# Kernel tuning notes

Measured on AMD Instinct MI355X. Metric: run time of the kernel, lower is better.

The kernel has to match this reference:

```python
import jax, jax.numpy as jnp
import numpy as np

B, T, D = 2, 2048, 1024
H = 16
HD = D // H  # 64


def setup_inputs() -> dict:
    key = jax.random.key(0)
    k1, k2, k3, k4, k5 = jax.random.split(key, 5)
    s = 0.02
    return {
        "x": jax.random.normal(k1, (B, T, D), dtype=jnp.float32),
        "Wqkv": jax.random.normal(k2, (D, 3 * D), dtype=jnp.float32) * s,
        "bqkv": jax.random.normal(k3, (3 * D,), dtype=jnp.float32) * s,
        "Wout": jax.random.normal(k4, (D, D), dtype=jnp.float32) * s,
        "bout": jax.random.normal(k5, (D,), dtype=jnp.float32) * s,
    }


def reference(x, Wqkv, bqkv, Wout, bout):
    b, t, c = x.shape
    qkv = (x @ Wqkv + bqkv).reshape(b, t, 3, H, HD)
    q = jnp.transpose(qkv[:, :, 0], (0, 2, 1, 3))  # [B,H,T,HD]
    k = jnp.transpose(qkv[:, :, 1], (0, 2, 1, 3))
    v = jnp.transpose(qkv[:, :, 2], (0, 2, 1, 3))
    att = jnp.einsum("bhqd,bhkd->bhqk", q, k) * (HD ** -0.5)
    mask = jnp.tril(jnp.ones((t, t), dtype=bool))  # causal, no past kv
    att = jnp.where(mask, att, -jnp.inf)
    att = jax.nn.softmax(att, axis=-1)
    y = jnp.einsum("bhqk,bhkd->bhqd", att, v)
    y = jnp.transpose(y, (0, 2, 1, 3)).reshape(b, t, c)
    return y @ Wout + bout
```

## Files before the change

kernel.cpp:

```cpp
#include <hip/hip_runtime.h>
#include <hip/hip_bf16.h>
#include <math.h>

#define B_  2
#define T_  2048
#define D_  1024
#define H_  16
#define HD_ 64

typedef __attribute__((ext_vector_type(8))) short short8;
typedef __attribute__((ext_vector_type(4))) float f32x4;

#if __has_builtin(__builtin_amdgcn_exp2f)
#define EXP2F __builtin_amdgcn_exp2f
#else
#define EXP2F exp2f
#endif

__device__ __forceinline__ ushort f2bf(float x) {
    unsigned u = __builtin_bit_cast(unsigned, x);
    return (ushort)((u + 0x7FFFu + ((u >> 16) & 1u)) >> 16);
}

__device__ __forceinline__ unsigned pack_bf2_fast(float a, float b) {
    unsigned ua = __builtin_bit_cast(unsigned, a) + 0x8000u;
    unsigned ub = __builtin_bit_cast(unsigned, b) + 0x8000u;
    return (ua >> 16) | (ub & 0xFFFF0000u);
}

__device__ __forceinline__ void load_lds_16B(const ushort* g, ushort* l) {
    __builtin_amdgcn_global_load_lds(
        (const __attribute__((address_space(1))) unsigned*)g,
        (__attribute__((address_space(3))) unsigned*)l, 16, 0, 0);
}

__global__ __launch_bounds__(256)
void prep_kernel(const float* __restrict__ x, ushort* __restrict__ xb,
                 const float* __restrict__ Wqkv, ushort* __restrict__ Wqkvt,
                 const float* __restrict__ Wout, ushort* __restrict__ Woutt)
{
    __shared__ ushort Ts[64][65];
    const int bid = blockIdx.x;

    if (bid < 512) {
        const int n4 = (B_ * T_ * D_) / 4;
        for (int i = bid * 256 + threadIdx.x; i < n4; i += 512 * 256) {
            float4 v = ((const float4*)x)[i];
            ushort4 o = { f2bf(v.x), f2bf(v.y), f2bf(v.z), f2bf(v.w) };
            ((ushort4*)xb)[i] = o;
        }
        return;
    }

    const float* W; ushort* Wt; int K, M, m0, k0;
    if (bid < 1280) {
        const int t = bid - 512;
        W = Wqkv; Wt = Wqkvt; K = D_; M = 3 * D_;
        m0 = (t % 48) * 64; k0 = (t / 48) * 64;
    } else {
        const int t = bid - 1280;
        W = Wout; Wt = Woutt; K = D_; M = D_;
        m0 = (t % 16) * 64; k0 = (t / 16) * 64;
    }

    const int tr = threadIdx.x >> 4;
    const int tc = threadIdx.x & 15;
    #pragma unroll
    for (int it = 0; it < 4; it++) {
        int k = tr + it * 16;
        float4 v = *(const float4*)&W[(size_t)(k0 + k) * M + m0 + tc * 4];
        Ts[tc * 4 + 0][k] = f2bf(v.x);
        Ts[tc * 4 + 1][k] = f2bf(v.y);
        Ts[tc * 4 + 2][k] = f2bf(v.z);
        Ts[tc * 4 + 3][k] = f2bf(v.w);
    }
    __syncthreads();
    #pragma unroll
    for (int it = 0; it < 2; it++) {
        const int mr  = (threadIdx.x >> 3) + it * 32;
        const int seg = (threadIdx.x & 7) * 8;
        short8 v;
        #pragma unroll
        for (int r = 0; r < 8; r++) v[r] = (short)Ts[mr][seg + r];
        *(short8*)&Wt[(size_t)(m0 + mr) * K + k0 + seg] = v;
    }
}

__global__ __launch_bounds__(256, 4)
void gemm_qkv(const ushort* __restrict__ A, const ushort* __restrict__ Bt,
              const float* __restrict__ bias,
              ushort* __restrict__ Qg, ushort* __restrict__ Kg,
              ushort* __restrict__ Vtg)
{
    const int K = D_;
    __shared__ __align__(16) ushort lds[16384];
    ushort* Asl = lds;
    ushort* Bsl = lds + 8192;

    const int tid = threadIdx.x;
    const int w  = tid >> 6, L = tid & 63;
    const int lt = L & 15, lq = L >> 4;
    const int wr = w >> 1, wc = w & 1;
    const int m0 = blockIdx.x * 128, n0 = blockIdx.y * 128;
    const int rsub = L >> 3;
    const int pgr  = L & 7;

    f32x4 acc[4][4] = {};

    for (int k0 = 0; k0 < K; k0 += 64) {
        __syncthreads();
        #pragma unroll
        for (int j = 0; j < 4; j++) {
            const int row  = (w * 4 + j) * 8 + rsub;
            const int gran = pgr ^ rsub;
            load_lds_16B(A  + (size_t)(n0 + row) * K + k0 + gran * 8,
                         &Asl[row * 64 + pgr * 8]);
            load_lds_16B(Bt + (size_t)(m0 + row) * K + k0 + gran * 8,
                         &Bsl[row * 64 + pgr * 8]);
        }
        __syncthreads();

        #pragma unroll
        for (int ks = 0; ks < 2; ks++) {
            short8 af[4], bf[4];
            #pragma unroll
            for (int i = 0; i < 4; i++) {
                const int ra = wr * 64 + i * 16 + lt;
                af[i] = *(const short8*)&Asl[ra * 64 + (((ks * 4 + lq) ^ (ra & 7)) * 8)];
                const int rb = wc * 64 + i * 16 + lt;
                bf[i] = *(const short8*)&Bsl[rb * 64 + (((ks * 4 + lq) ^ (rb & 7)) * 8)];
            }
            #pragma unroll
            for (int i = 0; i < 4; i++)
                #pragma unroll
                for (int j = 0; j < 4; j++)
                    acc[i][j] = __builtin_amdgcn_mfma_f32_16x16x32_bf16(af[i], bf[j], acc[i][j], 0, 0, 0);
        }
    }

    __syncthreads();
    const int s  = m0 >> 10;
    const int h0 = (m0 & 1023) >> 6;
    const float qs = (s == 0) ? 0.18033688011112042f : 1.0f;

    if (s < 2) {
        #pragma unroll
        for (int j = 0; j < 4; j++) {
            const int m  = wc * 64 + j * 16 + lt;
            const float bv = bias[m0 + m];
            #pragma unroll
            for (int i = 0; i < 4; i++) {
                const int n = wr * 64 + i * 16 + lq * 4;
                #pragma unroll
                for (int r = 0; r < 4; r++)
                    lds[(n + r) * 128 + m] = f2bf((acc[i][j][r] + bv) * qs);
            }
        }
        __syncthreads();
        ushort* dst = (s == 0 ? Qg : Kg);
        #pragma unroll
        for (int it = 0; it < 8; it++) {
            const int g   = tid + it * 256;
            const int row = g >> 4, c = g & 15;
            const int n = n0 + row;
            const int b = n >> 11, t = n & 2047;
            const int h = h0 + (c >> 3), d = (c & 7) * 8;
            short8 v = *(const short8*)&lds[row * 128 + c * 8];
            *(short8*)&dst[((size_t)(b * H_ + h) * T_ + t) * HD_ + d] = v;
        }
    } else {
        #pragma unroll
        for (int j = 0; j < 4; j++) {
            const int m  = wc * 64 + j * 16 + lt;
            const float bv = bias[m0 + m];
            #pragma unroll
            for (int i = 0; i < 4; i++) {
                const int n = wr * 64 + i * 16 + lq * 4;
                uint2 pk = { pack_bf2_fast(acc[i][j][0] + bv, acc[i][j][1] + bv),
                             pack_bf2_fast(acc[i][j][2] + bv, acc[i][j][3] + bv) };
                *(uint2*)&lds[m * 128 + n] = pk;
            }
        }
        __syncthreads();
        const int b = n0 >> 11, t0 = n0 & 2047;
        #pragma unroll
        for (int it = 0; it < 8; it++) {
            const int g   = tid + it * 256;
            const int row = g >> 4, c = g & 15;
            const int h = h0 + (row >> 6), d = row & 63;
            short8 v = *(const short8*)&lds[row * 128 + c * 8];
            *(short8*)&Vtg[((size_t)(b * H_ + h) * HD_ + d) * T_ + t0 + c * 8] = v;
        }
    }
}

__global__ __launch_bounds__(256, 4)
void gemm_out(const ushort* __restrict__ A, const ushort* __restrict__ Bt,
              const float* __restrict__ bias, float* __restrict__ C)
{
    const int K = D_, M = D_;
    __shared__ __align__(16) ushort lds[8192 + 4096];
    ushort* Asl = lds;
    ushort* Bsl = lds + 8192;

    const int tid = threadIdx.x;
    const int w  = tid >> 6, L = tid & 63;
    const int lt = L & 15, lq = L >> 4;
    const int wr = w >> 1, wc = w & 1;
    const int m0 = blockIdx.x * 64, n0 = blockIdx.y * 128;
    const int rsub = L >> 3;
    const int pgr  = L & 7;

    f32x4 acc[2][4] = {};

    for (int k0 = 0; k0 < K; k0 += 64) {
        __syncthreads();
        #pragma unroll
        for (int j = 0; j < 4; j++) {
            const int row  = (w * 4 + j) * 8 + rsub;
            const int gran = pgr ^ rsub;
            load_lds_16B(A + (size_t)(n0 + row) * K + k0 + gran * 8,
                         &Asl[row * 64 + pgr * 8]);
        }
        #pragma unroll
        for (int j = 0; j < 2; j++) {
            const int row  = (w * 2 + j) * 8 + rsub;
            const int gran = pgr ^ rsub;
            load_lds_16B(Bt + (size_t)(m0 + row) * K + k0 + gran * 8,
                         &Bsl[row * 64 + pgr * 8]);
        }
        __syncthreads();

        #pragma unroll
        for (int ks = 0; ks < 2; ks++) {
            short8 wf[2], yf[4];
            #pragma unroll
            for (int j = 0; j < 2; j++) {
                const int rb = wc * 32 + j * 16 + lt;
                wf[j] = *(const short8*)&Bsl[rb * 64 + (((ks * 4 + lq) ^ (rb & 7)) * 8)];
            }
            #pragma unroll
            for (int i = 0; i < 4; i++) {
                const int ra = wr * 64 + i * 16 + lt;
                yf[i] = *(const short8*)&Asl[ra * 64 + (((ks * 4 + lq) ^ (ra & 7)) * 8)];
            }
            #pragma unroll
            for (int j = 0; j < 2; j++)
                #pragma unroll
                for (int i = 0; i < 4; i++)
                    acc[j][i] = __builtin_amdgcn_mfma_f32_16x16x32_bf16(wf[j], yf[i], acc[j][i], 0, 0, 0);
        }
    }

    #pragma unroll
    for (int j = 0; j < 2; j++) {
        const int mbase = m0 + wc * 32 + j * 16 + lq * 4;
        const float4 bv = *(const float4*)&bias[mbase];
        #pragma unroll
        for (int i = 0; i < 4; i++) {
            const int n = n0 + wr * 64 + i * 16 + lt;
            float4 o = { acc[j][i][0] + bv.x, acc[j][i][1] + bv.y,
                         acc[j][i][2] + bv.z, acc[j][i][3] + bv.w };
            *(float4*)&C[(size_t)n * M + mbase] = o;
        }
    }
}

__global__ __launch_bounds__(256, 4)
void attn_mfma(const ushort* __restrict__ Qg, const ushort* __restrict__ Kg,
               const ushort* __restrict__ Vtg, ushort* __restrict__ yb)
{
    const int h = blockIdx.y, b = blockIdx.z;
    const int flip = ((blockIdx.y >> 3) ^ blockIdx.z) & 1;
    const int qb = flip ? blockIdx.x : (31 - blockIdx.x);
    const int tid = threadIdx.x;
    const int w  = tid >> 6, L = tid & 63;
    const int lt = L & 15, lq = L >> 4;
    const int kswz = lt & 7;

    __shared__ __align__(16) ushort Ks [128 * 64];
    __shared__ __align__(16) ushort Vts[64 * 128];
    __shared__ __align__(16) ushort Ps [4][16 * 40];

    const size_t bh = (size_t)(b * H_ + h);
    const ushort* Qbase  = Qg  + bh * T_ * HD_;
    const ushort* Kbase  = Kg  + bh * T_ * HD_;
    const ushort* Vtbase = Vtg + bh * HD_ * T_;

    const int q_glob = qb * 64 + w * 16 + lt;
    const short8 qf0 = *(const short8*)(Qbase + (size_t)q_glob * HD_ + lq * 8);
    const short8 qf1 = *(const short8*)(Qbase + (size_t)q_glob * HD_ + 32 + lq * 8);

    f32x4 acc_o[4] = {};
    float lsum = 0.f;

    const int krow = tid >> 3, kpg = tid & 7;
    const int vrow = tid >> 4, vpg = tid & 15;
    const int nk = (qb + 2) >> 1;

    for (int kb = 0; kb < nk; kb++) {
        __syncthreads();
        #pragma unroll
        for (int rr = 0; rr < 4; rr++) {
            const int row = krow + 32 * rr;
            load_lds_16B(Kbase + (size_t)(kb * 128 + row) * HD_ + (kpg ^ (row & 7)) * 8,
                         &Ks[row * 64 + kpg * 8]);
        }
        #pragma unroll
        for (int rr = 0; rr < 4; rr++) {
            const int d = vrow + 16 * rr;
            load_lds_16B(Vtbase + (size_t)d * T_ + kb * 128 + (vpg ^ (d & 7)) * 8,
                         &Vts[d * 128 + vpg * 8]);
        }
        __syncthreads();

        if (kb < nk - 1) {
            #pragma unroll
            for (int ks = 0; ks < 4; ks++) {
                const int row0 = (2 * ks) * 16 + lt;
                const int row1 = row0 + 16;
                short8 a00 = *(const short8*)&Ks[row0 * 64 + ((lq ^ kswz) * 8)];
                short8 a01 = *(const short8*)&Ks[row0 * 64 + (((4 + lq) ^ kswz) * 8)];
                short8 a10 = *(const short8*)&Ks[row1 * 64 + ((lq ^ kswz) * 8)];
                short8 a11 = *(const short8*)&Ks[row1 * 64 + (((4 + lq) ^ kswz) * 8)];
                f32x4 c0 = {}, c1 = {};
                c0 = __builtin_amdgcn_mfma_f32_16x16x32_bf16(a00, qf0, c0, 0, 0, 0);
                c0 = __builtin_amdgcn_mfma_f32_16x16x32_bf16(a01, qf1, c0, 0, 0, 0);
                c1 = __builtin_amdgcn_mfma_f32_16x16x32_bf16(a10, qf0, c1, 0, 0, 0);
                c1 = __builtin_amdgcn_mfma_f32_16x16x32_bf16(a11, qf1, c1, 0, 0, 0);

                float p0 = EXP2F(c0[0]), p1 = EXP2F(c0[1]);
                float p2 = EXP2F(c0[2]), p3 = EXP2F(c0[3]);
                float p4 = EXP2F(c1[0]), p5 = EXP2F(c1[1]);
                float p6 = EXP2F(c1[2]), p7 = EXP2F(c1[3]);
                lsum += ((p0 + p1) + (p2 + p3)) + ((p4 + p5) + (p6 + p7));
                uint2 pk0 = { pack_bf2_fast(p0, p1), pack_bf2_fast(p2, p3) };
                uint2 pk1 = { pack_bf2_fast(p4, p5), pack_bf2_fast(p6, p7) };
                *(uint2*)&Ps[w][lt * 40 + lq * 4]      = pk0;
                *(uint2*)&Ps[w][lt * 40 + 16 + lq * 4] = pk1;

                short8 pf = *(const short8*)&Ps[w][lt * 40 + lq * 8];

                #pragma unroll
                for (int dt = 0; dt < 4; dt++) {
                    const int vr = dt * 16 + lt;
                    short8 vf = *(const short8*)&Vts[vr * 128 + (((ks * 4 + lq) ^ kswz) * 8)];
                    acc_o[dt] = __builtin_amdgcn_mfma_f32_16x16x32_bf16(pf, vf, acc_o[dt], 0, 0, 0);
                }
            }
        } else {
            const int ksN = (qb & 1) ? 4 : 2;
            const int mk0 = (qb & 1) ? 2 : 0;
            for (int ks = 0; ks < ksN; ks++) {
                const int row0 = (2 * ks) * 16 + lt;
                const int row1 = row0 + 16;
                short8 a00 = *(const short8*)&Ks[row0 * 64 + ((lq ^ kswz) * 8)];
                short8 a01 = *(const short8*)&Ks[row0 * 64 + (((4 + lq) ^ kswz) * 8)];
                short8 a10 = *(const short8*)&Ks[row1 * 64 + ((lq ^ kswz) * 8)];
                short8 a11 = *(const short8*)&Ks[row1 * 64 + (((4 + lq) ^ kswz) * 8)];
                f32x4 c0 = {}, c1 = {};
                c0 = __builtin_amdgcn_mfma_f32_16x16x32_bf16(a00, qf0, c0, 0, 0, 0);
                c0 = __builtin_amdgcn_mfma_f32_16x16x32_bf16(a01, qf1, c0, 0, 0, 0);
                c1 = __builtin_amdgcn_mfma_f32_16x16x32_bf16(a10, qf0, c1, 0, 0, 0);
                c1 = __builtin_amdgcn_mfma_f32_16x16x32_bf16(a11, qf1, c1, 0, 0, 0);

                float p[8];
                #pragma unroll
                for (int r = 0; r < 4; r++) { p[r] = EXP2F(c0[r]); p[4 + r] = EXP2F(c1[r]); }
                if (ks >= mk0) {
                    const int key0 = kb * 128 + (2 * ks) * 16 + lq * 4;
                    #pragma unroll
                    for (int r = 0; r < 4; r++) {
                        if (key0 + r > q_glob)      p[r] = 0.f;
                        if (key0 + 16 + r > q_glob) p[4 + r] = 0.f;
                    }
                }
                lsum += ((p[0] + p[1]) + (p[2] + p[3])) + ((p[4] + p[5]) + (p[6] + p[7]));
                uint2 pk0 = { pack_bf2_fast(p[0], p[1]), pack_bf2_fast(p[2], p[3]) };
                uint2 pk1 = { pack_bf2_fast(p[4], p[5]), pack_bf2_fast(p[6], p[7]) };
                *(uint2*)&Ps[w][lt * 40 + lq * 4]      = pk0;
                *(uint2*)&Ps[w][lt * 40 + 16 + lq * 4] = pk1;

                short8 pf = *(const short8*)&Ps[w][lt * 40 + lq * 8];

                #pragma unroll
                for (int dt = 0; dt < 4; dt++) {
                    const int vr = dt * 16 + lt;
                    short8 vf = *(const short8*)&Vts[vr * 128 + (((ks * 4 + lq) ^ kswz) * 8)];
                    acc_o[dt] = __builtin_amdgcn_mfma_f32_16x16x32_bf16(pf, vf, acc_o[dt], 0, 0, 0);
                }
            }
        }
    }

    lsum += __shfl_xor(lsum, 16, 64);
    lsum += __shfl_xor(lsum, 32, 64);
    const float inv = 1.0f / lsum;

    float linv[4];
    #pragma unroll
    for (int r = 0; r < 4; r++) linv[r] = __shfl(inv, lq * 4 + r, 64);

    ushort* ybase = yb + (size_t)(b * T_ + qb * 64 + w * 16) * D_ + h * HD_;
    #pragma unroll
    for (int r = 0; r < 4; r++)
        #pragma unroll
        for (int dt = 0; dt < 4; dt++)
            ybase[(size_t)(lq * 4 + r) * D_ + dt * 16 + lt] = f2bf(acc_o[dt][r] * linv[r]);
}

extern "C" void kernel_launch(void* const* d_in, const int* in_sizes, int n_in,
                              void* d_out, int out_size, void* d_ws, size_t ws_size,
                              hipStream_t stream)
{
    const float* x    = (const float*)d_in[0];
    const float* Wqkv = (const float*)d_in[1];
    const float* bqkv = (const float*)d_in[2];
    const float* Wout = (const float*)d_in[3];
    const float* bout = (const float*)d_in[4];
    float* out = (float*)d_out;

    char* ws = (char*)d_ws;
    const size_t NT = (size_t)B_ * T_;
    ushort* xb     = (ushort*)ws;
    ushort* Wqkvt  = (ushort*)(ws + NT * D_ * 2);
    ushort* Woutt  = (ushort*)(ws + NT * D_ * 2 + (size_t)3 * D_ * D_ * 2);
    char*   p      = ws + NT * D_ * 2 + (size_t)4 * D_ * D_ * 2;
    const size_t qkv_elems = (size_t)B_ * H_ * T_ * HD_;
    ushort* Qg  = (ushort*)p;
    ushort* Kg  = (ushort*)(p + qkv_elems * 2);
    ushort* Vtg = (ushort*)(p + qkv_elems * 4);
    ushort* yb  = (ushort*)(p + qkv_elems * 6);

    prep_kernel<<<1536, 256, 0, stream>>>(x, xb, Wqkv, Wqkvt, Wout, Woutt);

    gemm_qkv<<<dim3(3 * D_ / 128, NT / 128), 256, 0, stream>>>(
        xb, Wqkvt, bqkv, Qg, Kg, Vtg);

    attn_mfma<<<dim3(32, H_, B_), 256, 0, stream>>>(Qg, Kg, Vtg, yb);

    gemm_out<<<dim3(D_ / 64, NT / 128), 256, 0, stream>>>(
        yb, Woutt, bout, out);
}
```

Before: 168.9 us.

## Process 128 query rows per attention block to reuse K/V tiles

Each attention block now covers 128 query rows instead of 64, with every wavefront handling two 16-row query sub-tiles. Each K/V tile staged in LDS therefore feeds twice as many MFMAs, halving the global K/V traffic and barrier count per query. The P scratch buffer is double-buffered per sub-tile and the diagonal block uses per-sub-tile causal masking. The cost is higher register pressure (launch bounds lowered to 2 blocks), half as many blocks (512) and a coarser load-balancing flip between batches.

```diff
diff --git a/kernel.cpp b/kernel.cpp
--- a/kernel.cpp
+++ b/kernel.cpp
@@ -266,13 +266,12 @@
     }
 }
 
-__global__ __launch_bounds__(256, 4)
+__global__ __launch_bounds__(256, 2)
 void attn_mfma(const ushort* __restrict__ Qg, const ushort* __restrict__ Kg,
                const ushort* __restrict__ Vtg, ushort* __restrict__ yb)
 {
     const int h = blockIdx.y, b = blockIdx.z;
-    const int flip = ((blockIdx.y >> 3) ^ blockIdx.z) & 1;
-    const int qb = flip ? blockIdx.x : (31 - blockIdx.x);
+    const int Qt = blockIdx.z ? blockIdx.x : (15 - blockIdx.x);
     const int tid = threadIdx.x;
     const int w  = tid >> 6, L = tid & 63;
     const int lt = L & 15, lq = L >> 4;
@@ -280,23 +279,27 @@
 
     __shared__ __align__(16) ushort Ks [128 * 64];
     __shared__ __align__(16) ushort Vts[64 * 128];
-    __shared__ __align__(16) ushort Ps [4][16 * 40];
+    __shared__ __align__(16) ushort Ps [4][2][2][640];
 
     const size_t bh = (size_t)(b * H_ + h);
     const ushort* Qbase  = Qg  + bh * T_ * HD_;
     const ushort* Kbase  = Kg  + bh * T_ * HD_;
     const ushort* Vtbase = Vtg + bh * HD_ * T_;
 
-    const int q_glob = qb * 64 + w * 16 + lt;
-    const short8 qf0 = *(const short8*)(Qbase + (size_t)q_glob * HD_ + lq * 8);
-    const short8 qf1 = *(const short8*)(Qbase + (size_t)q_glob * HD_ + 32 + lq * 8);
-
-    f32x4 acc_o[4] = {};
-    float lsum = 0.f;
+    short8 qf[2][2];
+    #pragma unroll
+    for (int s = 0; s < 2; s++) {
+        const int row = Qt * 128 + w * 32 + s * 16 + lt;
+        qf[s][0] = *(const short8*)(Qbase + (size_t)row * HD_ + lq * 8);
+        qf[s][1] = *(const short8*)(Qbase + (size_t)row * HD_ + 32 + lq * 8);
+    }
+
+    f32x4 acc_o[2][4] = {};
+    float lsum[2] = {0.f, 0.f};
 
     const int krow = tid >> 3, kpg = tid & 7;
     const int vrow = tid >> 4, vpg = tid & 15;
-    const int nk = (qb + 2) >> 1;
+    const int nk = Qt + 1;
 
     for (int kb = 0; kb < nk; kb++) {
         __syncthreads();
@@ -323,90 +326,111 @@
                 short8 a01 = *(const short8*)&Ks[row0 * 64 + (((4 + lq) ^ kswz) * 8)];
                 short8 a10 = *(const short8*)&Ks[row1 * 64 + ((lq ^ kswz) * 8)];
                 short8 a11 = *(const short8*)&Ks[row1 * 64 + (((4 + lq) ^ kswz) * 8)];
-                f32x4 c0 = {}, c1 = {};
-                c0 = __builtin_amdgcn_mfma_f32_16x16x32_bf16(a00, qf0, c0, 0, 0, 0);
-                c0 = __builtin_amdgcn_mfma_f32_16x16x32_bf16(a01, qf1, c0, 0, 0, 0);
-                c1 = __builtin_amdgcn_mfma_f32_16x16x32_bf16(a10, qf0, c1, 0, 0, 0);
-                c1 = __builtin_amdgcn_mfma_f32_16x16x32_bf16(a11, qf1, c1, 0, 0, 0);
-
-                float p0 = EXP2F(c0[0]), p1 = EXP2F(c0[1]);
-                float p2 = EXP2F(c0[2]), p3 = EXP2F(c0[3]);
-                float p4 = EXP2F(c1[0]), p5 = EXP2F(c1[1]);
-                float p6 = EXP2F(c1[2]), p7 = EXP2F(c1[3]);
-                lsum += ((p0 + p1) + (p2 + p3)) + ((p4 + p5) + (p6 + p7));
-                uint2 pk0 = { pack_bf2_fast(p0, p1), pack_bf2_fast(p2, p3) };
-                uint2 pk1 = { pack_bf2_fast(p4, p5), pack_bf2_fast(p6, p7) };
-                *(uint2*)&Ps[w][lt * 40 + lq * 4]      = pk0;
-                *(uint2*)&Ps[w][lt * 40 + 16 + lq * 4] = pk1;
-
-                short8 pf = *(const short8*)&Ps[w][lt * 40 + lq * 8];
+                f32x4 c00 = {}, c01 = {}, c10 = {}, c11 = {};
+                c00 = __builtin_amdgcn_mfma_f32_16x16x32_bf16(a00, qf[0][0], c00, 0, 0, 0);
+                c00 = __builtin_amdgcn_mfma_f32_16x16x32_bf16(a01, qf[0][1], c00, 0, 0, 0);
+                c01 = __builtin_amdgcn_mfma_f32_16x16x32_bf16(a10, qf[0][0], c01, 0, 0, 0);
+                c01 = __builtin_amdgcn_mfma_f32_16x16x32_bf16(a11, qf[0][1], c01, 0, 0, 0);
+                c10 = __builtin_amdgcn_mfma_f32_16x16x32_bf16(a00, qf[1][0], c10, 0, 0, 0);
+                c10 = __builtin_amdgcn_mfma_f32_16x16x32_bf16(a01, qf[1][1], c10, 0, 0, 0);
+                c11 = __builtin_amdgcn_mfma_f32_16x16x32_bf16(a10, qf[1][0], c11, 0, 0, 0);
+                c11 = __builtin_amdgcn_mfma_f32_16x16x32_bf16(a11, qf[1][1], c11, 0, 0, 0);
+
+                float p0 = EXP2F(c00[0]), p1 = EXP2F(c00[1]), p2 = EXP2F(c00[2]), p3 = EXP2F(c00[3]);
+                float p4 = EXP2F(c01[0]), p5 = EXP2F(c01[1]), p6 = EXP2F(c01[2]), p7 = EXP2F(c01[3]);
+                lsum[0] += ((p0 + p1) + (p2 + p3)) + ((p4 + p5) + (p6 + p7));
+                *(uint2*)&Ps[w][0][ks & 1][lt * 40 + lq * 4] =
+                    (uint2){ pack_bf2_fast(p0, p1), pack_bf2_fast(p2, p3) };
+                *(uint2*)&Ps[w][0][ks & 1][lt * 40 + 16 + lq * 4] =
+                    (uint2){ pack_bf2_fast(p4, p5), pack_bf2_fast(p6, p7) };
+
+                float r0 = EXP2F(c10[0]), r1 = EXP2F(c10[1]), r2 = EXP2F(c10[2]), r3 = EXP2F(c10[3]);
+                float r4 = EXP2F(c11[0]), r5 = EXP2F(c11[1]), r6 = EXP2F(c11[2]), r7 = EXP2F(c11[3]);
+                lsum[1] += ((r0 + r1) + (r2 + r3)) + ((r4 + r5) + (r6 + r7));
+                *(uint2*)&Ps[w][1][ks & 1][lt * 40 + lq * 4] =
+                    (uint2){ pack_bf2_fast(r0, r1), pack_bf2_fast(r2, r3) };
+                *(uint2*)&Ps[w][1][ks & 1][lt * 40 + 16 + lq * 4] =
+                    (uint2){ pack_bf2_fast(r4, r5), pack_bf2_fast(r6, r7) };
+
+                short8 pf0 = *(const short8*)&Ps[w][0][ks & 1][lt * 40 + lq * 8];
+                short8 pf1 = *(const short8*)&Ps[w][1][ks & 1][lt * 40 + lq * 8];
 
                 #pragma unroll
                 for (int dt = 0; dt < 4; dt++) {
                     const int vr = dt * 16 + lt;
                     short8 vf = *(const short8*)&Vts[vr * 128 + (((ks * 4 + lq) ^ kswz) * 8)];
-                    acc_o[dt] = __builtin_amdgcn_mfma_f32_16x16x32_bf16(pf, vf, acc_o[dt], 0, 0, 0);
+                    acc_o[0][dt] = __builtin_amdgcn_mfma_f32_16x16x32_bf16(pf0, vf, acc_o[0][dt], 0, 0, 0);
+                    acc_o[1][dt] = __builtin_amdgcn_mfma_f32_16x16x32_bf16(pf1, vf, acc_o[1][dt], 0, 0, 0);
                 }
             }
         } else {
-            const int ksN = (qb & 1) ? 4 : 2;
-            const int mk0 = (qb & 1) ? 2 : 0;
-            for (int ks = 0; ks < ksN; ks++) {
-                const int row0 = (2 * ks) * 16 + lt;
-                const int row1 = row0 + 16;
-                short8 a00 = *(const short8*)&Ks[row0 * 64 + ((lq ^ kswz) * 8)];
-                short8 a01 = *(const short8*)&Ks[row0 * 64 + (((4 + lq) ^ kswz) * 8)];
-                short8 a10 = *(const short8*)&Ks[row1 * 64 + ((lq ^ kswz) * 8)];
-                short8 a11 = *(const short8*)&Ks[row1 * 64 + (((4 + lq) ^ kswz) * 8)];
-                f32x4 c0 = {}, c1 = {};
-                c0 = __builtin_amdgcn_mfma_f32_16x16x32_bf16(a00, qf0, c0, 0, 0, 0);
-                c0 = __builtin_amdgcn_mfma_f32_16x16x32_bf16(a01, qf1, c0, 0, 0, 0);
-                c1 = __builtin_amdgcn_mfma_f32_16x16x32_bf16(a10, qf0, c1, 0, 0, 0);
-                c1 = __builtin_amdgcn_mfma_f32_16x16x32_bf16(a11, qf1, c1, 0, 0, 0);
-
-                float p[8];
-                #pragma unroll
-                for (int r = 0; r < 4; r++) { p[r] = EXP2F(c0[r]); p[4 + r] = EXP2F(c1[r]); }
-                if (ks >= mk0) {
-                    const int key0 = kb * 128 + (2 * ks) * 16 + lq * 4;
+            #pragma unroll
+            for (int s = 0; s < 2; s++) {
+                const int row_base = w * 32 + s * 16;
+                const int mk  = row_base >> 5;
+                const int ksN = (row_base + 47) >> 5;
+                const int q_in = row_base + lt;
+                for (int ks = 0; ks < ksN; ks++) {
+                    const int row0 = (2 * ks) * 16 + lt;
+                    const int row1 = row0 + 16;
+                    short8 a00 = *(const short8*)&Ks[row0 * 64 + ((lq ^ kswz) * 8)];
+                    short8 a01 = *(const short8*)&Ks[row0 * 64 + (((4 + lq) ^ kswz) * 8)];
+                    short8 a10 = *(const short8*)&Ks[row1 * 64 + ((lq ^ kswz) * 8)];
+                    short8 a11 = *(const short8*)&Ks[row1 * 64 + (((4 + lq) ^ kswz) * 8)];
+                    f32x4 c0 = {}, c1 = {};
+                    c0 = __builtin_amdgcn_mfma_f32_16x16x32_bf16(a00, qf[s][0], c0, 0, 0, 0);
+                    c0 = __builtin_amdgcn_mfma_f32_16x16x32_bf16(a01, qf[s][1], c0, 0, 0, 0);
+                    c1 = __builtin_amdgcn_mfma_f32_16x16x32_bf16(a10, qf[s][0], c1, 0, 0, 0);
+                    c1 = __builtin_amdgcn_mfma_f32_16x16x32_bf16(a11, qf[s][1], c1, 0, 0, 0);
+
+                    float p[8];
                     #pragma unroll
-                    for (int r = 0; r < 4; r++) {
-                        if (key0 + r > q_glob)      p[r] = 0.f;
-                        if (key0 + 16 + r > q_glob) p[4 + r] = 0.f;
+                    for (int r = 0; r < 4; r++) { p[r] = EXP2F(c0[r]); p[4 + r] = EXP2F(c1[r]); }
+                    if (ks >= mk) {
+                        const int key0 = ks * 32 + lq * 4;
+                        #pragma unroll
+                        for (int r = 0; r < 4; r++) {
+                            if (key0 + r > q_in)      p[r] = 0.f;
+                            if (key0 + 16 + r > q_in) p[4 + r] = 0.f;
+                        }
+                    }
+                    lsum[s] += ((p[0] + p[1]) + (p[2] + p[3])) + ((p[4] + p[5]) + (p[6] + p[7]));
+                    *(uint2*)&Ps[w][s][ks & 1][lt * 40 + lq * 4] =
+                        (uint2){ pack_bf2_fast(p[0], p[1]), pack_bf2_fast(p[2], p[3]) };
+                    *(uint2*)&Ps[w][s][ks & 1][lt * 40 + 16 + lq * 4] =
+                        (uint2){ pack_bf2_fast(p[4], p[5]), pack_bf2_fast(p[6], p[7]) };
+
+                    short8 pf = *(const short8*)&Ps[w][s][ks & 1][lt * 40 + lq * 8];
+
+                    #pragma unroll
+                    for (int dt = 0; dt < 4; dt++) {
+                        const int vr = dt * 16 + lt;
+                        short8 vf = *(const short8*)&Vts[vr * 128 + (((ks * 4 + lq) ^ kswz) * 8)];
+                        acc_o[s][dt] = __builtin_amdgcn_mfma_f32_16x16x32_bf16(pf, vf, acc_o[s][dt], 0, 0, 0);
                     }
                 }
-                lsum += ((p[0] + p[1]) + (p[2] + p[3])) + ((p[4] + p[5]) + (p[6] + p[7]));
-                uint2 pk0 = { pack_bf2_fast(p[0], p[1]), pack_bf2_fast(p[2], p[3]) };
-                uint2 pk1 = { pack_bf2_fast(p[4], p[5]), pack_bf2_fast(p[6], p[7]) };
-                *(uint2*)&Ps[w][lt * 40 + lq * 4]      = pk0;
-                *(uint2*)&Ps[w][lt * 40 + 16 + lq * 4] = pk1;
-
-                short8 pf = *(const short8*)&Ps[w][lt * 40 + lq * 8];
-
-                #pragma unroll
-                for (int dt = 0; dt < 4; dt++) {
-                    const int vr = dt * 16 + lt;
-                    short8 vf = *(const short8*)&Vts[vr * 128 + (((ks * 4 + lq) ^ kswz) * 8)];
-                    acc_o[dt] = __builtin_amdgcn_mfma_f32_16x16x32_bf16(pf, vf, acc_o[dt], 0, 0, 0);
-                }
-            }
-        }
-    }
-
-    lsum += __shfl_xor(lsum, 16, 64);
-    lsum += __shfl_xor(lsum, 32, 64);
-    const float inv = 1.0f / lsum;
-
-    float linv[4];
+            }
+        }
+    }
+
     #pragma unroll
-    for (int r = 0; r < 4; r++) linv[r] = __shfl(inv, lq * 4 + r, 64);
-
-    ushort* ybase = yb + (size_t)(b * T_ + qb * 64 + w * 16) * D_ + h * HD_;
-    #pragma unroll
-    for (int r = 0; r < 4; r++)
-        #pragma unroll
-        for (int dt = 0; dt < 4; dt++)
-            ybase[(size_t)(lq * 4 + r) * D_ + dt * 16 + lt] = f2bf(acc_o[dt][r] * linv[r]);
+    for (int s = 0; s < 2; s++) {
+        float ls = lsum[s];
+        ls += __shfl_xor(ls, 16, 64);
+        ls += __shfl_xor(ls, 32, 64);
+        const float inv = 1.0f / ls;
+
+        float linv[4];
+        #pragma unroll
+        for (int r = 0; r < 4; r++) linv[r] = __shfl(inv, lq * 4 + r, 64);
+
+        ushort* ybase = yb + (size_t)(b * T_ + Qt * 128 + w * 32 + s * 16) * D_ + h * HD_;
+        #pragma unroll
+        for (int r = 0; r < 4; r++)
+            #pragma unroll
+            for (int dt = 0; dt < 4; dt++)
+                ybase[(size_t)(lq * 4 + r) * D_ + dt * 16 + lt] = f2bf(acc_o[s][dt][r] * linv[r]);
+    }
 }
 
 extern "C" void kernel_launch(void* const* d_in, const int* in_sizes, int n_in,
@@ -437,7 +461,7 @@
     gemm_qkv<<<dim3(3 * D_ / 128, NT / 128), 256, 0, stream>>>(
         xb, Wqkvt, bqkv, Qg, Kg, Vtg);
 
-    attn_mfma<<<dim3(32, H_, B_), 256, 0, stream>>>(Qg, Kg, Vtg, yb);
+    attn_mfma<<<dim3(16, H_, B_), 256, 0, stream>>>(Qg, Kg, Vtg, yb);
 
     gemm_out<<<dim3(D_ / 64, NT / 128), 256, 0, stream>>>(
         yb, Woutt, bout, out);
```

New measurement: 172.2 us. No clear change (+1.9%).

## Split attention KV range across two wave groups with LDS merge

Applied to the files above, without the earlier changes.

The attention block grows to 512 threads, split into two halves of four waves. Each half processes a disjoint part of the causal key range in 64-key tiles, and the partial outputs and row sums are then merged through LDS before normalisation. This is meant to shorten the serial KV loop per block and raise the number of waves in flight. In exchange it adds an extra LDS reduction and extra barriers. The halves can also be imbalanced: the upper half is idle on some iterations but still waits at the barriers.

```diff
diff --git a/kernel.cpp b/kernel.cpp
--- a/kernel.cpp
+++ b/kernel.cpp
@@ -266,7 +266,7 @@
     }
 }
 
-__global__ __launch_bounds__(256, 4)
+__global__ __launch_bounds__(512, 6)
 void attn_mfma(const ushort* __restrict__ Qg, const ushort* __restrict__ Kg,
                const ushort* __restrict__ Vtg, ushort* __restrict__ yb)
 {
@@ -274,139 +274,135 @@
     const int flip = ((blockIdx.y >> 3) ^ blockIdx.z) & 1;
     const int qb = flip ? blockIdx.x : (31 - blockIdx.x);
     const int tid = threadIdx.x;
-    const int w  = tid >> 6, L = tid & 63;
+    const int w    = tid >> 6;
+    const int half = w >> 2;
+    const int sw   = w & 3;
+    const int L  = tid & 63;
     const int lt = L & 15, lq = L >> 4;
-    const int kswz = lt & 7;
-
-    __shared__ __align__(16) ushort Ks [128 * 64];
-    __shared__ __align__(16) ushort Vts[64 * 128];
-    __shared__ __align__(16) ushort Ps [4][16 * 40];
+
+    __shared__ __align__(16) ushort Ks [2][64 * 64];
+    __shared__ __align__(16) ushort Vts[2][64 * 64];
+    __shared__ __align__(16) ushort Ps [8][640];
 
     const size_t bh = (size_t)(b * H_ + h);
     const ushort* Qbase  = Qg  + bh * T_ * HD_;
     const ushort* Kbase  = Kg  + bh * T_ * HD_;
     const ushort* Vtbase = Vtg + bh * HD_ * T_;
 
-    const int q_glob = qb * 64 + w * 16 + lt;
+    const int q_in   = sw * 16 + lt;
+    const int q_glob = qb * 64 + q_in;
     const short8 qf0 = *(const short8*)(Qbase + (size_t)q_glob * HD_ + lq * 8);
     const short8 qf1 = *(const short8*)(Qbase + (size_t)q_glob * HD_ + 32 + lq * 8);
 
     f32x4 acc_o[4] = {};
     float lsum = 0.f;
 
-    const int krow = tid >> 3, kpg = tid & 7;
-    const int vrow = tid >> 4, vpg = tid & 15;
-    const int nk = (qb + 2) >> 1;
-
-    for (int kb = 0; kb < nk; kb++) {
-        __syncthreads();
-        #pragma unroll
-        for (int rr = 0; rr < 4; rr++) {
-            const int row = krow + 32 * rr;
-            load_lds_16B(Kbase + (size_t)(kb * 128 + row) * HD_ + (kpg ^ (row & 7)) * 8,
-                         &Ks[row * 64 + kpg * 8]);
-        }
-        #pragma unroll
-        for (int rr = 0; rr < 4; rr++) {
-            const int d = vrow + 16 * rr;
-            load_lds_16B(Vtbase + (size_t)d * T_ + kb * 128 + (vpg ^ (d & 7)) * 8,
-                         &Vts[d * 128 + vpg * 8]);
-        }
-        __syncthreads();
-
-        if (kb < nk - 1) {
-            #pragma unroll
-            for (int ks = 0; ks < 4; ks++) {
-                const int row0 = (2 * ks) * 16 + lt;
-                const int row1 = row0 + 16;
-                short8 a00 = *(const short8*)&Ks[row0 * 64 + ((lq ^ kswz) * 8)];
-                short8 a01 = *(const short8*)&Ks[row0 * 64 + (((4 + lq) ^ kswz) * 8)];
-                short8 a10 = *(const short8*)&Ks[row1 * 64 + ((lq ^ kswz) * 8)];
-                short8 a11 = *(const short8*)&Ks[row1 * 64 + (((4 + lq) ^ kswz) * 8)];
-                f32x4 c0 = {}, c1 = {};
-                c0 = __builtin_amdgcn_mfma_f32_16x16x32_bf16(a00, qf0, c0, 0, 0, 0);
-                c0 = __builtin_amdgcn_mfma_f32_16x16x32_bf16(a01, qf1, c0, 0, 0, 0);
-                c1 = __builtin_amdgcn_mfma_f32_16x16x32_bf16(a10, qf0, c1, 0, 0, 0);
-                c1 = __builtin_amdgcn_mfma_f32_16x16x32_bf16(a11, qf1, c1, 0, 0, 0);
-
-                float p0 = EXP2F(c0[0]), p1 = EXP2F(c0[1]);
-                float p2 = EXP2F(c0[2]), p3 = EXP2F(c0[3]);
-                float p4 = EXP2F(c1[0]), p5 = EXP2F(c1[1]);
-                float p6 = EXP2F(c1[2]), p7 = EXP2F(c1[3]);
-                lsum += ((p0 + p1) + (p2 + p3)) + ((p4 + p5) + (p6 + p7));
-                uint2 pk0 = { pack_bf2_fast(p0, p1), pack_bf2_fast(p2, p3) };
-                uint2 pk1 = { pack_bf2_fast(p4, p5), pack_bf2_fast(p6, p7) };
-                *(uint2*)&Ps[w][lt * 40 + lq * 4]      = pk0;
-                *(uint2*)&Ps[w][lt * 40 + 16 + lq * 4] = pk1;
-
-                short8 pf = *(const short8*)&Ps[w][lt * 40 + lq * 8];
-
+    const int nk = qb + 1;
+    const int n0 = nk >> 1;
+    const int iters   = nk - n0;
+    const int kb_base = half ? n0 : 0;
+    const int kb_cnt  = half ? (nk - n0) : n0;
+
+    const int ht = tid & 255;
+    const int srow = ht >> 3, spg = ht & 7;
+
+    for (int i = 0; i < iters; i++) {
+        const bool active = (i < kb_cnt);
+        const int kb = kb_base + i;
+        __syncthreads();
+        if (active) {
+            #pragma unroll
+            for (int rr = 0; rr < 2; rr++) {
+                const int row = srow + 32 * rr;
+                load_lds_16B(Kbase + (size_t)(kb * 64 + row) * HD_ + (spg ^ (row & 7)) * 8,
+                             &Ks[half][row * 64 + spg * 8]);
+            }
+            #pragma unroll
+            for (int rr = 0; rr < 2; rr++) {
+                const int d = srow + 32 * rr;
+                load_lds_16B(Vtbase + (size_t)d * T_ + kb * 64 + (spg ^ (d & 7)) * 8,
+                             &Vts[half][d * 64 + spg * 8]);
+            }
+        }
+        __syncthreads();
+        if (!active) continue;
+
+        const bool diag = (kb == qb);
+        const int ksN = diag ? (1 + (sw >> 1)) : 2;
+        const int mkc = diag ? (sw >> 1) : 2;
+
+        for (int ks = 0; ks < ksN; ks++) {
+            const int row0 = (2 * ks) * 16 + lt;
+            const int row1 = row0 + 16;
+            short8 a00 = *(const short8*)&Ks[half][row0 * 64 + ((lq ^ (row0 & 7)) * 8)];
+            short8 a01 = *(const short8*)&Ks[half][row0 * 64 + (((4 + lq) ^ (row0 & 7)) * 8)];
+            short8 a10 = *(const short8*)&Ks[half][row1 * 64 + ((lq ^ (row1 & 7)) * 8)];
+            short8 a11 = *(const short8*)&Ks[half][row1 * 64 + (((4 + lq) ^ (row1 & 7)) * 8)];
+            f32x4 c0 = {}, c1 = {};
+            c0 = __builtin_amdgcn_mfma_f32_16x16x32_bf16(a00, qf0, c0, 0, 0, 0);
+            c0 = __builtin_amdgcn_mfma_f32_16x16x32_bf16(a01, qf1, c0, 0, 0, 0);
+            c1 = __builtin_amdgcn_mfma_f32_16x16x32_bf16(a10, qf0, c1, 0, 0, 0);
+            c1 = __builtin_amdgcn_mfma_f32_16x16x32_bf16(a11, qf1, c1, 0, 0, 0);
+
+            float p[8];
+            #pragma unroll
+            for (int r = 0; r < 4; r++) { p[r] = EXP2F(c0[r]); p[4 + r] = EXP2F(c1[r]); }
+            if (ks == mkc) {
+                const int key0 = ks * 32 + lq * 4;
                 #pragma unroll
-                for (int dt = 0; dt < 4; dt++) {
-                    const int vr = dt * 16 + lt;
-                    short8 vf = *(const short8*)&Vts[vr * 128 + (((ks * 4 + lq) ^ kswz) * 8)];
-                    acc_o[dt] = __builtin_amdgcn_mfma_f32_16x16x32_bf16(pf, vf, acc_o[dt], 0, 0, 0);
+                for (int r = 0; r < 4; r++) {
+                    if (key0 + r > q_in)      p[r] = 0.f;
+                    if (key0 + 16 + r > q_in) p[4 + r] = 0.f;
                 }
             }
-        } else {
-            const int ksN = (qb & 1) ? 4 : 2;
-            const int mk0 = (qb & 1) ? 2 : 0;
-            for (int ks = 0; ks < ksN; ks++) {
-                const int row0 = (2 * ks) * 16 + lt;
-                const int row1 = row0 + 16;
-                short8 a00 = *(const short8*)&Ks[row0 * 64 + ((lq ^ kswz) * 8)];
-                short8 a01 = *(const short8*)&Ks[row0 * 64 + (((4 + lq) ^ kswz) * 8)];
-                short8 a10 = *(const short8*)&Ks[row1 * 64 + ((lq ^ kswz) * 8)];
-                short8 a11 = *(const short8*)&Ks[row1 * 64 + (((4 + lq) ^ kswz) * 8)];
-                f32x4 c0 = {}, c1 = {};
-                c0 = __builtin_amdgcn_mfma_f32_16x16x32_bf16(a00, qf0, c0, 0, 0, 0);
-                c0 = __builtin_amdgcn_mfma_f32_16x16x32_bf16(a01, qf1, c0, 0, 0, 0);
-                c1 = __builtin_amdgcn_mfma_f32_16x16x32_bf16(a10, qf0, c1, 0, 0, 0);
-                c1 = __builtin_amdgcn_mfma_f32_16x16x32_bf16(a11, qf1, c1, 0, 0, 0);
-
-                float p[8];
-                #pragma unroll
-                for (int r = 0; r < 4; r++) { p[r] = EXP2F(c0[r]); p[4 + r] = EXP2F(c1[r]); }
-                if (ks >= mk0) {
-                    const int key0 = kb * 128 + (2 * ks) * 16 + lq * 4;
-                    #pragma unroll
-                    for (int r = 0; r < 4; r++) {
-                        if (key0 + r > q_glob)      p[r] = 0.f;
-                        if (key0 + 16 + r > q_glob) p[4 + r] = 0.f;
-                    }
-                }
-                lsum += ((p[0] + p[1]) + (p[2] + p[3])) + ((p[4] + p[5]) + (p[6] + p[7]));
-                uint2 pk0 = { pack_bf2_fast(p[0], p[1]), pack_bf2_fast(p[2], p[3]) };
-                uint2 pk1 = { pack_bf2_fast(p[4], p[5]), pack_bf2_fast(p[6], p[7]) };
-                *(uint2*)&Ps[w][lt * 40 + lq * 4]      = pk0;
-                *(uint2*)&Ps[w][lt * 40 + 16 + lq * 4] = pk1;
-
-                short8 pf = *(const short8*)&Ps[w][lt * 40 + lq * 8];
-
-                #pragma unroll
-                for (int dt = 0; dt < 4; dt++) {
-                    const int vr = dt * 16 + lt;
-                    short8 vf = *(const short8*)&Vts[vr * 128 + (((ks * 4 + lq) ^ kswz) * 8)];
-                    acc_o[dt] = __builtin_amdgcn_mfma_f32_16x16x32_bf16(pf, vf, acc_o[dt], 0, 0, 0);
-                }
+            lsum += ((p[0] + p[1]) + (p[2] + p[3])) + ((p[4] + p[5]) + (p[6] + p[7]));
+            *(uint2*)&Ps[w][lt * 40 + lq * 4] =
+                (uint2){ pack_bf2_fast(p[0], p[1]), pack_bf2_fast(p[2], p[3]) };
+            *(uint2*)&Ps[w][lt * 40 + 16 + lq * 4] =
+                (uint2){ pack_bf2_fast(p[4], p[5]), pack_bf2_fast(p[6], p[7]) };
+
+            short8 pf = *(const short8*)&Ps[w][lt * 40 + lq * 8];
+
+            #pragma unroll
+            for (int dt = 0; dt < 4; dt++) {
+                const int vr = dt * 16 + lt;
+                short8 vf = *(const short8*)&Vts[half][vr * 64 + (((ks * 4 + lq) ^ (vr & 7)) * 8)];
+                acc_o[dt] = __builtin_amdgcn_mfma_f32_16x16x32_bf16(pf, vf, acc_o[dt], 0, 0, 0);
             }
         }
     }
 
     lsum += __shfl_xor(lsum, 16, 64);
     lsum += __shfl_xor(lsum, 32, 64);
-    const float inv = 1.0f / lsum;
-
-    float linv[4];
-    #pragma unroll
-    for (int r = 0; r < 4; r++) linv[r] = __shfl(inv, lq * 4 + r, 64);
-
-    ushort* ybase = yb + (size_t)(b * T_ + qb * 64 + w * 16) * D_ + h * HD_;
-    #pragma unroll
-    for (int r = 0; r < 4; r++)
+
+    __syncthreads();
+    float* Of = (float*)&Ks[0][0];
+    float* Lf = (float*)&Vts[0][0];
+    if (half == 1) {
         #pragma unroll
         for (int dt = 0; dt < 4; dt++)
-            ybase[(size_t)(lq * 4 + r) * D_ + dt * 16 + lt] = f2bf(acc_o[dt][r] * linv[r]);
+            #pragma unroll
+            for (int r = 0; r < 4; r++)
+                Of[sw * 1024 + (lq * 4 + r) * 64 + dt * 16 + lt] = acc_o[dt][r];
+        if (lq == 0) Lf[sw * 16 + lt] = lsum;
+    }
+    __syncthreads();
+    if (half == 0) {
+        const float invl = 1.0f / (lsum + Lf[sw * 16 + lt]);
+        float linv[4];
+        #pragma unroll
+        for (int r = 0; r < 4; r++) linv[r] = __shfl(invl, lq * 4 + r, 64);
+
+        ushort* ybase = yb + (size_t)(b * T_ + qb * 64 + sw * 16) * D_ + h * HD_;
+        #pragma unroll
+        for (int r = 0; r < 4; r++)
+            #pragma unroll
+            for (int dt = 0; dt < 4; dt++) {
+                float o = acc_o[dt][r] +
+                          Of[sw * 1024 + (lq * 4 + r) * 64 + dt * 16 + lt];
+                ybase[(size_t)(lq * 4 + r) * D_ + dt * 16 + lt] = f2bf(o * linv[r]);
+            }
+    }
 }
 
 extern "C" void kernel_launch(void* const* d_in, const int* in_sizes, int n_in,
@@ -437,7 +433,7 @@
     gemm_qkv<<<dim3(3 * D_ / 128, NT / 128), 256, 0, stream>>>(
         xb, Wqkvt, bqkv, Qg, Kg, Vtg);
 
-    attn_mfma<<<dim3(32, H_, B_), 256, 0, stream>>>(Qg, Kg, Vtg, yb);
+    attn_mfma<<<dim3(32, H_, B_), 512, 0, stream>>>(Qg, Kg, Vtg, yb);
 
     gemm_out<<<dim3(D_ / 64, NT / 128), 256, 0, stream>>>(
         yb, Woutt, bout, out);
```

Measured after the change: 180.0 us. 1.07x slower.

## Load V fragments directly from global memory instead of staging in LDS

Applied to the files above, without the earlier changes.

Removes the shared-memory staging of the transposed V tile. Each lane now reads its V MFMA operands straight from global memory (expected to hit L2) at the start of every 32-key step, and the separate full and last-block loops are merged into one loop with computed bounds. This cuts LDS traffic and footprint, which may allow more resident blocks. The cost is that all four waves of a block re-read the same V data from global memory, exposing global-load latency inside the inner loop, and the unified loop may unroll less well.

```diff
diff --git a/kernel.cpp b/kernel.cpp
--- a/kernel.cpp
+++ b/kernel.cpp
@@ -276,16 +276,14 @@
     const int tid = threadIdx.x;
     const int w  = tid >> 6, L = tid & 63;
     const int lt = L & 15, lq = L >> 4;
-    const int kswz = lt & 7;
-
-    __shared__ __align__(16) ushort Ks [128 * 64];
-    __shared__ __align__(16) ushort Vts[64 * 128];
-    __shared__ __align__(16) ushort Ps [4][16 * 40];
+
+    __shared__ __align__(16) ushort Ks[128 * 64];
+    __shared__ __align__(16) ushort Ps[4][640];
 
     const size_t bh = (size_t)(b * H_ + h);
     const ushort* Qbase  = Qg  + bh * T_ * HD_;
     const ushort* Kbase  = Kg  + bh * T_ * HD_;
-    const ushort* Vtbase = Vtg + bh * HD_ * T_;
+    const ushort* Vf     = Vtg + bh * HD_ * T_ + (size_t)lt * T_ + lq * 8;
 
     const int q_glob = qb * 64 + w * 16 + lt;
     const short8 qf0 = *(const short8*)(Qbase + (size_t)q_glob * HD_ + lq * 8);
@@ -295,7 +293,6 @@
     float lsum = 0.f;
 
     const int krow = tid >> 3, kpg = tid & 7;
-    const int vrow = tid >> 4, vpg = tid & 15;
     const int nk = (qb + 2) >> 1;
 
     for (int kb = 0; kb < nk; kb++) {
@@ -306,90 +303,55 @@
             load_lds_16B(Kbase + (size_t)(kb * 128 + row) * HD_ + (kpg ^ (row & 7)) * 8,
                          &Ks[row * 64 + kpg * 8]);
         }
-        #pragma unroll
-        for (int rr = 0; rr < 4; rr++) {
-            const int d = vrow + 16 * rr;
-            load_lds_16B(Vtbase + (size_t)d * T_ + kb * 128 + (vpg ^ (d & 7)) * 8,
-                         &Vts[d * 128 + vpg * 8]);
-        }
-        __syncthreads();
-
-        if (kb < nk - 1) {
-            #pragma unroll
-            for (int ks = 0; ks < 4; ks++) {
-                const int row0 = (2 * ks) * 16 + lt;
-                const int row1 = row0 + 16;
-                short8 a00 = *(const short8*)&Ks[row0 * 64 + ((lq ^ kswz) * 8)];
-                short8 a01 = *(const short8*)&Ks[row0 * 64 + (((4 + lq) ^ kswz) * 8)];
-                short8 a10 = *(const short8*)&Ks[row1 * 64 + ((lq ^ kswz) * 8)];
-                short8 a11 = *(const short8*)&Ks[row1 * 64 + (((4 + lq) ^ kswz) * 8)];
-                f32x4 c0 = {}, c1 = {};
-                c0 = __builtin_amdgcn_mfma_f32_16x16x32_bf16(a00, qf0, c0, 0, 0, 0);
-                c0 = __builtin_amdgcn_mfma_f32_16x16x32_bf16(a01, qf1, c0, 0, 0, 0);
-                c1 = __builtin_amdgcn_mfma_f32_16x16x32_bf16(a10, qf0, c1, 0, 0, 0);
-                c1 = __builtin_amdgcn_mfma_f32_16x16x32_bf16(a11, qf1, c1, 0, 0, 0);
-
-                float p0 = EXP2F(c0[0]), p1 = EXP2F(c0[1]);
-                float p2 = EXP2F(c0[2]), p3 = EXP2F(c0[3]);
-                float p4 = EXP2F(c1[0]), p5 = EXP2F(c1[1]);
-                float p6 = EXP2F(c1[2]), p7 = EXP2F(c1[3]);
-                lsum += ((p0 + p1) + (p2 + p3)) + ((p4 + p5) + (p6 + p7));
-                uint2 pk0 = { pack_bf2_fast(p0, p1), pack_bf2_fast(p2, p3) };
-                uint2 pk1 = { pack_bf2_fast(p4, p5), pack_bf2_fast(p6, p7) };
-                *(uint2*)&Ps[w][lt * 40 + lq * 4]      = pk0;
-                *(uint2*)&Ps[w][lt * 40 + 16 + lq * 4] = pk1;
-
-                short8 pf = *(const short8*)&Ps[w][lt * 40 + lq * 8];
-
+        __syncthreads();
+
+        const bool last = (kb == nk - 1);
+        const int ksN = (!last || (qb & 1)) ? 4 : 2;
+        const int mk0 = last ? ((qb & 1) ? 2 : 0) : 4;
+
+        for (int ks = 0; ks < ksN; ks++) {
+            const int key0 = kb * 128 + ks * 32;
+            const ushort* vp = Vf + key0;
+            short8 vf0 = *(const short8*)(vp);
+            short8 vf1 = *(const short8*)(vp + 16 * T_);
+            short8 vf2 = *(const short8*)(vp + 32 * T_);
+            short8 vf3 = *(const short8*)(vp + 48 * T_);
+
+            const int row0 = (2 * ks) * 16 + lt;
+            const int row1 = row0 + 16;
+            short8 a00 = *(const short8*)&Ks[row0 * 64 + ((lq ^ (row0 & 7)) * 8)];
+            short8 a01 = *(const short8*)&Ks[row0 * 64 + (((4 + lq) ^ (row0 & 7)) * 8)];
+            short8 a10 = *(const short8*)&Ks[row1 * 64 + ((lq ^ (row1 & 7)) * 8)];
+            short8 a11 = *(const short8*)&Ks[row1 * 64 + (((4 + lq) ^ (row1 & 7)) * 8)];
+            f32x4 c0 = {}, c1 = {};
+            c0 = __builtin_amdgcn_mfma_f32_16x16x32_bf16(a00, qf0, c0, 0, 0, 0);
+            c0 = __builtin_amdgcn_mfma_f32_16x16x32_bf16(a01, qf1, c0, 0, 0, 0);
+            c1 = __builtin_amdgcn_mfma_f32_16x16x32_bf16(a10, qf0, c1, 0, 0, 0);
+            c1 = __builtin_amdgcn_mfma_f32_16x16x32_bf16(a11, qf1, c1, 0, 0, 0);
+
+            float p[8];
+            #pragma unroll
+            for (int r = 0; r < 4; r++) { p[r] = EXP2F(c0[r]); p[4 + r] = EXP2F(c1[r]); }
+            if (ks >= mk0) {
+                const int kq = key0 + lq * 4;
                 #pragma unroll
-                for (int dt = 0; dt < 4; dt++) {
-                    const int vr = dt * 16 + lt;
-                    short8 vf = *(const short8*)&Vts[vr * 128 + (((ks * 4 + lq) ^ kswz) * 8)];
-                    acc_o[dt] = __builtin_amdgcn_mfma_f32_16x16x32_bf16(pf, vf, acc_o[dt], 0, 0, 0);
+                for (int r = 0; r < 4; r++) {
+                    if (kq + r > q_glob)      p[r] = 0.f;
+                    if (kq + 16 + r > q_glob) p[4 + r] = 0.f;
                 }
             }
-        } else {
-            const int ksN = (qb & 1) ? 4 : 2;
-            const int mk0 = (qb & 1) ? 2 : 0;
-            for (int ks = 0; ks < ksN; ks++) {
-                const int row0 = (2 * ks) * 16 + lt;
-                const int row1 = row0 + 16;
-                short8 a00 = *(const short8*)&Ks[row0 * 64 + ((lq ^ kswz) * 8)];
-                short8 a01 = *(const short8*)&Ks[row0 * 64 + (((4 + lq) ^ kswz) * 8)];
-                short8 a10 = *(const short8*)&Ks[row1 * 64 + ((lq ^ kswz) * 8)];
-                short8 a11 = *(const short8*)&Ks[row1 * 64 + (((4 + lq) ^ kswz) * 8)];
-                f32x4 c0 = {}, c1 = {};
-                c0 = __builtin_amdgcn_mfma_f32_16x16x32_bf16(a00, qf0, c0, 0, 0, 0);
-                c0 = __builtin_amdgcn_mfma_f32_16x16x32_bf16(a01, qf1, c0, 0, 0, 0);
-                c1 = __builtin_amdgcn_mfma_f32_16x16x32_bf16(a10, qf0, c1, 0, 0, 0);
-                c1 = __builtin_amdgcn_mfma_f32_16x16x32_bf16(a11, qf1, c1, 0, 0, 0);
-
-                float p[8];
-                #pragma unroll
-                for (int r = 0; r < 4; r++) { p[r] = EXP2F(c0[r]); p[4 + r] = EXP2F(c1[r]); }
-                if (ks >= mk0) {
-                    const int key0 = kb * 128 + (2 * ks) * 16 + lq * 4;
-                    #pragma unroll
-                    for (int r = 0; r < 4; r++) {
-                        if (key0 + r > q_glob)      p[r] = 0.f;
-                        if (key0 + 16 + r > q_glob) p[4 + r] = 0.f;
-                    }
-                }
-                lsum += ((p[0] + p[1]) + (p[2] + p[3])) + ((p[4] + p[5]) + (p[6] + p[7]));
-                uint2 pk0 = { pack_bf2_fast(p[0], p[1]), pack_bf2_fast(p[2], p[3]) };
-                uint2 pk1 = { pack_bf2_fast(p[4], p[5]), pack_bf2_fast(p[6], p[7]) };
-                *(uint2*)&Ps[w][lt * 40 + lq * 4]      = pk0;
-                *(uint2*)&Ps[w][lt * 40 + 16 + lq * 4] = pk1;
-
-                short8 pf = *(const short8*)&Ps[w][lt * 40 + lq * 8];
-
-                #pragma unroll
-                for (int dt = 0; dt < 4; dt++) {
-                    const int vr = dt * 16 + lt;
-                    short8 vf = *(const short8*)&Vts[vr * 128 + (((ks * 4 + lq) ^ kswz) * 8)];
-                    acc_o[dt] = __builtin_amdgcn_mfma_f32_16x16x32_bf16(pf, vf, acc_o[dt], 0, 0, 0);
-                }
-            }
+            lsum += ((p[0] + p[1]) + (p[2] + p[3])) + ((p[4] + p[5]) + (p[6] + p[7]));
+            *(uint2*)&Ps[w][lt * 40 + lq * 4] =
+                (uint2){ pack_bf2_fast(p[0], p[1]), pack_bf2_fast(p[2], p[3]) };
+            *(uint2*)&Ps[w][lt * 40 + 16 + lq * 4] =
+                (uint2){ pack_bf2_fast(p[4], p[5]), pack_bf2_fast(p[6], p[7]) };
+
+            short8 pf = *(const short8*)&Ps[w][lt * 40 + lq * 8];
+
+            acc_o[0] = __builtin_amdgcn_mfma_f32_16x16x32_bf16(pf, vf0, acc_o[0], 0, 0, 0);
+            acc_o[1] = __builtin_amdgcn_mfma_f32_16x16x32_bf16(pf, vf1, acc_o[1], 0, 0, 0);
+            acc_o[2] = __builtin_amdgcn_mfma_f32_16x16x32_bf16(pf, vf2, acc_o[2], 0, 0, 0);
+            acc_o[3] = __builtin_amdgcn_mfma_f32_16x16x32_bf16(pf, vf3, acc_o[3], 0, 0, 0);
         }
     }
 
```

Result: slower. 197.9 us (+17.1%).
